# Kernel tuning notes

Measured on AMD Instinct MI355X. Metric: run time of the kernel, lower is better.

## Reference

```python
import jax, jax.numpy as jnp
import numpy as np

B, T, E, H = 2, 2048, 1024, 16
HD = E // H
EPS = 1e-5


def layer_norm(x, g, b):
    mu = jnp.mean(x, axis=-1, keepdims=True)
    var = jnp.mean(jnp.square(x - mu), axis=-1, keepdims=True)
    return (x - mu) * jax.lax.rsqrt(var + EPS) * g + b


def setup_inputs() -> dict:
    key = jax.random.key(0)
    ks = jax.random.split(key, 12)
    s = 0.02
    return {
        "x": jax.random.normal(ks[0], (B, T, E), jnp.float32),
        "Wk": jax.random.normal(ks[1], (E, E), jnp.float32) * s,
        "Wq": jax.random.normal(ks[2], (E, E), jnp.float32) * s,
        "Wv": jax.random.normal(ks[3], (E, E), jnp.float32) * s,
        "Wp": jax.random.normal(ks[4], (E, E), jnp.float32) * s,
        "bp": jnp.zeros((E,), jnp.float32),
        "W1": jax.random.normal(ks[5], (E, 4 * E), jnp.float32) * s,
        "b1": jnp.zeros((4 * E,), jnp.float32),
        "W2": jax.random.normal(ks[6], (4 * E, E), jnp.float32) * s,
        "b2": jnp.zeros((E,), jnp.float32),
        "g1": jnp.ones((E,), jnp.float32),
        "be1": jnp.zeros((E,), jnp.float32),
        "g2": jnp.ones((E,), jnp.float32),
        "be2": jnp.zeros((E,), jnp.float32),
    }


def reference(x, Wk, Wq, Wv, Wp, bp, W1, b1, W2, b2, g1, be1, g2, be2):
    # --- attention sublayer ---
    h = layer_norm(x, g1, be1)
    q = (h @ Wq).reshape(B, T, H, HD).transpose(0, 2, 1, 3)  # [B,H,T,HD]
    k = (h @ Wk).reshape(B, T, H, HD).transpose(0, 2, 1, 3)
    v = (h @ Wv).reshape(B, T, H, HD).transpose(0, 2, 1, 3)
    scores = jnp.einsum('bhqd,bhkd->bhqk', q, k) * (HD ** -0.5)
    causal = jnp.tril(jnp.ones((T, T), bool))
    scores = jnp.where(causal, scores, -jnp.inf)
    probs = jax.nn.softmax(scores, axis=-1)  # dropout is identity (eval)
    attn = jnp.einsum('bhqk,bhkd->bhqd', probs, v)
    attn = attn.transpose(0, 2, 1, 3).reshape(B, T, E)
    x = x + attn @ Wp + bp
    # --- FFN sublayer ---
    h2 = layer_norm(x, g2, be2)
    ff = jax.nn.relu(h2 @ W1 + b1) @ W2 + b2
    return x + ff
```

## Files before the change

### kernel.cpp

```cpp
#include <hip/hip_runtime.h>
#include <hip/hip_bf16.h>

#define B_ 2
#define T_ 2048
#define E_ 1024
#define H_ 16
#define HD_ 64
#define NT (B_*T_)

typedef __attribute__((ext_vector_type(8))) short s16x8;
typedef __attribute__((ext_vector_type(4))) float f32x4;
typedef __attribute__((ext_vector_type(4))) unsigned int u32x4;

using bf16 = __hip_bfloat16;

#define MFMA16(a,b,c) __builtin_amdgcn_mfma_f32_16x16x32_bf16(a,b,c,0,0,0)

__device__ inline unsigned short f2bf(float f) {
    bf16 h = __float2bfloat16(f);
    return *reinterpret_cast<unsigned short*>(&h);
}

__device__ __forceinline__ void async_cp16(const void* g, void* l) {
    __builtin_amdgcn_global_load_lds((const __attribute__((address_space(1))) void*)g,
                                     (__attribute__((address_space(3))) void*)l,
                                     16, 0, 0);
}

__global__ __launch_bounds__(256) void transpose_cvt4(const float* __restrict__ W0,
                                                      const float* __restrict__ W1,
                                                      const float* __restrict__ W2,
                                                      const float* __restrict__ W3,
                                                      bf16* __restrict__ Wt) {
    __shared__ float tile[32][33];
    int tx = threadIdx.x, ty = threadIdx.y;
    int z = blockIdx.z;
    const float* W = z == 0 ? W0 : z == 1 ? W1 : z == 2 ? W2 : W3;
    bf16* dst = Wt + (size_t)z * 1024 * 1024;
    int n0 = blockIdx.x * 32, k0 = blockIdx.y * 32;
#pragma unroll
    for (int i = 0; i < 4; ++i)
        tile[ty + i*8][tx] = W[(size_t)(k0 + ty + i*8)*1024 + n0 + tx];
    __syncthreads();
#pragma unroll
    for (int i = 0; i < 4; ++i)
        dst[(size_t)(n0 + ty + i*8)*1024 + k0 + tx] = __float2bfloat16(tile[tx][ty + i*8]);
}

__global__ __launch_bounds__(256) void transpose_cvt(const float* __restrict__ W,
                                                     bf16* __restrict__ Wt,
                                                     int K, int N) {
    __shared__ float tile[32][33];
    int tx = threadIdx.x, ty = threadIdx.y;
    int n0 = blockIdx.x * 32, k0 = blockIdx.y * 32;
#pragma unroll
    for (int i = 0; i < 4; ++i)
        tile[ty + i*8][tx] = W[(size_t)(k0 + ty + i*8)*N + n0 + tx];
    __syncthreads();
#pragma unroll
    for (int i = 0; i < 4; ++i)
        Wt[(size_t)(n0 + ty + i*8)*K + k0 + tx] = __float2bfloat16(tile[tx][ty + i*8]);
}

__global__ __launch_bounds__(256) void ln_kernel(const float* __restrict__ x,
                                                 const float* __restrict__ g,
                                                 const float* __restrict__ b,
                                                 bf16* __restrict__ h) {
    int row = blockIdx.x;
    int tid = threadIdx.x;
    const float4 xv = *reinterpret_cast<const float4*>(x + (size_t)row*E_ + tid*4);
    float s  = xv.x + xv.y + xv.z + xv.w;
    float sq = xv.x*xv.x + xv.y*xv.y + xv.z*xv.z + xv.w*xv.w;
#pragma unroll
    for (int o = 32; o > 0; o >>= 1) { s += __shfl_xor(s, o); sq += __shfl_xor(sq, o); }
    __shared__ float red[8];
    int w = tid >> 6, lane = tid & 63;
    if (lane == 0) { red[w] = s; red[4 + w] = sq; }
    __syncthreads();
    float S = red[0] + red[1] + red[2] + red[3];
    float Q = red[4] + red[5] + red[6] + red[7];
    float mu = S * (1.0f/E_);
    float var = Q * (1.0f/E_) - mu*mu;
    float rs = rsqrtf(var + 1e-5f);
    const float4 gv = *reinterpret_cast<const float4*>(g + tid*4);
    const float4 bv = *reinterpret_cast<const float4*>(b + tid*4);
    ushort4 o4;
    o4.x = f2bf((xv.x - mu)*rs*gv.x + bv.x);
    o4.y = f2bf((xv.y - mu)*rs*gv.y + bv.y);
    o4.z = f2bf((xv.z - mu)*rs*gv.z + bv.z);
    o4.w = f2bf((xv.w - mu)*rs*gv.w + bv.w);
    *reinterpret_cast<ushort4*>(h + (size_t)row*E_ + tid*4) = o4;
}

template<int BN, int EPI>
__global__ __launch_bounds__(256)
void gemm_t(const bf16* __restrict__ A, const bf16* __restrict__ Bt, void* Cout,
            const float* __restrict__ bias, const float* res,
            int M, int N, int K) {
    constexpr int NB = BN / 32;
    constexpr int HALF = BN / 2;
    __shared__ bf16 As[128*64];
    __shared__ bf16 Bs[BN*64];
    int tid = threadIdx.x;
    int lane = tid & 63, w = tid >> 6;
    int wr = w >> 1, wc = w & 1;
    int m0 = blockIdx.y * 128, n0 = blockIdx.x * BN;
    int lr = lane & 15, lq = lane >> 4;
    f32x4 acc[4][NB] = {};
    int srow = w*8 + (lane >> 3);
    int schunk = ((lane & 7) ^ (srow & 7)) * 8;
    const bf16* Ap = A  + (size_t)(m0 + srow)*K + schunk;
    const bf16* Bp = Bt + (size_t)(n0 + srow)*K + schunk;
    for (int k0 = 0; k0 < K; k0 += 64) {
#pragma unroll
        for (int i = 0; i < 4; ++i)
            async_cp16(Ap + (size_t)(i*32)*K + k0, (char*)As + i*4096 + w*1024);
#pragma unroll
        for (int i = 0; i < BN/32; ++i)
            async_cp16(Bp + (size_t)(i*32)*K + k0, (char*)Bs + i*4096 + w*1024);
        __syncthreads();
        const char* Asb = (const char*)As;
        const char* Bsb = (const char*)Bs;
        s16x8 af[2][4], bfr[2][NB];
#pragma unroll
        for (int m = 0; m < 4; ++m) {
            int row = wr*64 + m*16 + lr;
            int base = row*128, sw = (row & 7) << 4;
#pragma unroll
            for (int kk = 0; kk < 2; ++kk)
                af[kk][m] = *reinterpret_cast<const s16x8*>(Asb + base + ((kk*64 + lq*16) ^ sw));
        }
#pragma unroll
        for (int n = 0; n < NB; ++n) {
            int row = wc*HALF + n*16 + lr;
            int base = row*128, sw = (row & 7) << 4;
#pragma unroll
            for (int kk = 0; kk < 2; ++kk)
                bfr[kk][n] = *reinterpret_cast<const s16x8*>(Bsb + base + ((kk*64 + lq*16) ^ sw));
        }
        __builtin_amdgcn_s_setprio(1);
#pragma unroll
        for (int kk = 0; kk < 2; ++kk)
#pragma unroll
            for (int m = 0; m < 4; ++m)
#pragma unroll
                for (int n = 0; n < NB; ++n)
                    acc[m][n] = MFMA16(af[kk][m], bfr[kk][n], acc[m][n]);
        __builtin_amdgcn_s_setprio(0);
        __syncthreads();
    }
#pragma unroll
    for (int m = 0; m < 4; ++m) {
#pragma unroll
        for (int n = 0; n < NB; ++n) {
            int col = n0 + wc*HALF + n*16 + lr;
#pragma unroll
            for (int r = 0; r < 4; ++r) {
                int row = m0 + wr*64 + m*16 + lq*4 + r;
                float v = acc[m][n][r];
                if (EPI == 0) {
                    reinterpret_cast<bf16*>(Cout)[(size_t)row*N + col] = __float2bfloat16(v);
                } else if (EPI == 1) {
                    reinterpret_cast<float*>(Cout)[(size_t)row*N + col] =
                        v + bias[col] + res[(size_t)row*N + col];
                } else {
                    v += bias[col];
                    v = v > 0.f ? v : 0.f;
                    reinterpret_cast<bf16*>(Cout)[(size_t)row*N + col] = __float2bfloat16(v);
                }
            }
        }
    }
}

__global__ __launch_bounds__(256) void v_transpose(const bf16* __restrict__ qkv,
                                                   bf16* __restrict__ Vt) {
    __shared__ unsigned short tile[32][33];
    int tx = threadIdx.x, ty = threadIdx.y;
    int bh = blockIdx.z;
    int b = bh >> 4, h = bh & 15;
    int t0 = blockIdx.x * 32, d0 = blockIdx.y * 32;
    const unsigned short* src = reinterpret_cast<const unsigned short*>(qkv);
#pragma unroll
    for (int i = 0; i < 4; ++i)
        tile[ty + i*8][tx] = src[(size_t)(b*T_ + t0 + ty + i*8)*3072 + 2048 + h*64 + d0 + tx];
    __syncthreads();
    unsigned short* dst = reinterpret_cast<unsigned short*>(Vt);
#pragma unroll
    for (int i = 0; i < 4; ++i)
        dst[(size_t)(bh*64 + d0 + ty + i*8)*T_ + t0 + tx] = tile[tx][ty + i*8];
}

__global__ __launch_bounds__(256)
void flash_attn(const bf16* __restrict__ qkv, const bf16* __restrict__ Vt,
                bf16* __restrict__ O) {
    __shared__ char smem[40960];
    int tid = threadIdx.x;
    int lane = tid & 63, w = tid >> 6;
    int lr = lane & 15, lq = lane >> 4;
    int bh = blockIdx.y, b = bh >> 4, h = bh & 15;
    int qt = (int)((blockIdx.x + blockIdx.y) & 31);
    int q0 = qt * 64;
    int qw = q0 + w * 16;
    const bf16* Qb = qkv + (size_t)(b*T_)*3072 + h*HD_;
    const bf16* Kb = Qb + 1024;
    const bf16* Vb = Vt + (size_t)bh * HD_ * T_;
    char* Pw = smem + 32768 + w*2048;

    int sc_   = (((lane & 7) ^ ((lane >> 3) & 7))) * 8;
    int srow_ = w*8 + (lane >> 3);

    s16x8 qf[2];
#pragma unroll
    for (int kk = 0; kk < 2; ++kk)
        qf[kk] = *reinterpret_cast<const s16x8*>(Qb + (size_t)(qw + lr)*3072 + kk*32 + lq*8);
    f32x4 od[4] = {};
    float mrun = -1e30f, lrun = 0.f;
    const float SLOG2E = 0.125f * 1.44269504088896f;
    int ntiles = qt + 1;

#define STAGE(bufi, tile) do {                                                          \
        int kv0s_ = (tile) * 64;                                                        \
        _Pragma("unroll")                                                               \
        for (int i_ = 0; i_ < 2; ++i_) {                                                \
            int rr_ = i_*32 + srow_;                                                    \
            async_cp16(Kb + (size_t)(kv0s_ + rr_)*3072 + sc_,                           \
                       smem + (bufi)*8192 + i_*4096 + w*1024);                          \
            async_cp16(Vb + (size_t)rr_*2048 + kv0s_ + sc_,                             \
                       smem + 16384 + (bufi)*8192 + i_*4096 + w*1024);                  \
        } } while (0)

    STAGE(0, 0);
    for (int it = 0; it < ntiles; ++it) {
        int curb = it & 1;
        int kv0 = it * 64;
        if (it + 1 < ntiles) {
            STAGE(curb ^ 1, it + 1);
            asm volatile("s_waitcnt vmcnt(4)" ::: "memory");
        } else {
            asm volatile("s_waitcnt vmcnt(0)" ::: "memory");
        }
        __builtin_amdgcn_sched_barrier(0);
        __builtin_amdgcn_s_barrier();
        __builtin_amdgcn_sched_barrier(0);
        const char* Kt = smem + curb*8192;
        const char* Vtl = smem + 16384 + curb*8192;
        f32x4 sc[4];
        __builtin_amdgcn_s_setprio(1);
#pragma unroll
        for (int n = 0; n < 4; ++n) {
            int row = n*16 + lr;
            s16x8 kf0 = *reinterpret_cast<const s16x8*>(Kt + row*128 + ((lq ^ (row&7)) << 4));
            s16x8 kf1 = *reinterpret_cast<const s16x8*>(Kt + row*128 + (((4+lq) ^ (row&7)) << 4));
            f32x4 z = {0.f, 0.f, 0.f, 0.f};
            z = MFMA16(kf0, qf[0], z);
            z = MFMA16(kf1, qf[1], z);
            sc[n] = z;
        }
        __builtin_amdgcn_s_setprio(0);
        if (it == ntiles - 1) {
            int q = qw + lr;
#pragma unroll
            for (int n = 0; n < 4; ++n)
#pragma unroll
                for (int r = 0; r < 4; ++r)
                    if (kv0 + n*16 + lq*4 + r > q) sc[n][r] = -1e30f;
        }
        float mx01 = fmaxf(fmaxf(sc[0][0], sc[0][1]), fmaxf(sc[0][2], sc[0][3]));
        float mx1  = fmaxf(fmaxf(sc[1][0], sc[1][1]), fmaxf(sc[1][2], sc[1][3]));
        float mx2  = fmaxf(fmaxf(sc[2][0], sc[2][1]), fmaxf(sc[2][2], sc[2][3]));
        float mx3  = fmaxf(fmaxf(sc[3][0], sc[3][1]), fmaxf(sc[3][2], sc[3][3]));
        float pmax = fmaxf(fmaxf(mx01, mx1), fmaxf(mx2, mx3));
        pmax = fmaxf(pmax, __shfl_xor(pmax, 16));
        pmax = fmaxf(pmax, __shfl_xor(pmax, 32));
        float ps = pmax * SLOG2E;
        if (__ballot(ps > mrun + 8.f)) {
            float mn = fmaxf(mrun, ps);
            float corr = exp2f(mrun - mn);
            mrun = mn;
            lrun *= corr;
            float cR[4];
#pragma unroll
            for (int r = 0; r < 4; ++r) cR[r] = __shfl(corr, lq*4 + r);
#pragma unroll
            for (int nd = 0; nd < 4; ++nd)
#pragma unroll
                for (int r = 0; r < 4; ++r)
                    od[nd][r] *= cR[r];
        }
        float psum = 0.f;
#pragma unroll
        for (int n = 0; n < 4; ++n) {
            float p0 = exp2f(fmaf(sc[n][0], SLOG2E, -mrun));
            float p1 = exp2f(fmaf(sc[n][1], SLOG2E, -mrun));
            float p2 = exp2f(fmaf(sc[n][2], SLOG2E, -mrun));
            float p3 = exp2f(fmaf(sc[n][3], SLOG2E, -mrun));
            psum += (p0 + p1) + (p2 + p3);
            uint2 pk;
            pk.x = ((unsigned)f2bf(p1) << 16) | f2bf(p0);
            pk.y = ((unsigned)f2bf(p3) << 16) | f2bf(p2);
            int bo = (lr*128 + n*32 + lq*8) ^ ((lr & 7) << 4);
            *reinterpret_cast<uint2*>(Pw + bo) = pk;
        }
        psum += __shfl_xor(psum, 16);
        psum += __shfl_xor(psum, 32);
        lrun += psum;
        asm volatile("" ::: "memory");
        s16x8 pa[2];
#pragma unroll
        for (int kk = 0; kk < 2; ++kk) {
            int bo = (lr*128 + kk*64 + lq*16) ^ ((lr & 7) << 4);
            pa[kk] = *reinterpret_cast<const s16x8*>(Pw + bo);
        }
        __builtin_amdgcn_s_setprio(1);
#pragma unroll
        for (int nd = 0; nd < 4; ++nd) {
            int row = nd*16 + lr;
            s16x8 vf0 = *reinterpret_cast<const s16x8*>(Vtl + row*128 + ((lq ^ (row&7)) << 4));
            s16x8 vf1 = *reinterpret_cast<const s16x8*>(Vtl + row*128 + (((4+lq) ^ (row&7)) << 4));
            od[nd] = MFMA16(pa[0], vf0, od[nd]);
            od[nd] = MFMA16(pa[1], vf1, od[nd]);
        }
        __builtin_amdgcn_s_setprio(0);
        __builtin_amdgcn_sched_barrier(0);
        __builtin_amdgcn_s_barrier();
        __builtin_amdgcn_sched_barrier(0);
    }
#undef STAGE
    float lR[4];
#pragma unroll
    for (int r = 0; r < 4; ++r) lR[r] = 1.0f / __shfl(lrun, lq*4 + r);
#pragma unroll
    for (int nd = 0; nd < 4; ++nd) {
#pragma unroll
        for (int r = 0; r < 4; ++r) {
            int row = qw + lq*4 + r;
            O[(size_t)(b*T_ + row)*E_ + h*HD_ + nd*16 + lr] = __float2bfloat16(od[nd][r] * lR[r]);
        }
    }
}

extern "C" void kernel_launch(void* const* d_in, const int* in_sizes, int n_in,
                              void* d_out, int out_size, void* d_ws, size_t ws_size,
                              hipStream_t stream) {
    const float* x   = (const float*)d_in[0];
    const float* Wk  = (const float*)d_in[1];
    const float* Wq  = (const float*)d_in[2];
    const float* Wv  = (const float*)d_in[3];
    const float* Wp  = (const float*)d_in[4];
    const float* bp  = (const float*)d_in[5];
    const float* W1  = (const float*)d_in[6];
    const float* b1  = (const float*)d_in[7];
    const float* W2  = (const float*)d_in[8];
    const float* b2  = (const float*)d_in[9];
    const float* g1  = (const float*)d_in[10];
    const float* be1 = (const float*)d_in[11];
    const float* g2  = (const float*)d_in[12];
    const float* be2 = (const float*)d_in[13];
    float* out = (float*)d_out;

    char* ws = (char*)d_ws;
    bf16* Wqkv_t = (bf16*)(ws + 0);
    bf16* Wp_t   = (bf16*)(ws + 6291456);
    bf16* W1_t   = (bf16*)(ws + 8388608);
    bf16* W2_t   = (bf16*)(ws + 16777216);
    bf16* h      = (bf16*)(ws + 25165824);
    bf16* qkv    = (bf16*)(ws + 33554432);
    bf16* Vt     = (bf16*)(ws + 58720256);
    bf16* attnO  = (bf16*)(ws + 67108864);
    bf16* ff1    = (bf16*)(ws + 33554432);
    float* x2    = (ws_size >= 92274688) ? (float*)(ws + 75497472) : out;

    dim3 tb(32, 8);
    transpose_cvt4<<<dim3(32, 32, 4), tb, 0, stream>>>(Wq, Wk, Wv, Wp, Wqkv_t);
    transpose_cvt<<<dim3(128, 32), tb, 0, stream>>>(W1, W1_t, 1024, 4096);
    transpose_cvt<<<dim3(32, 128), tb, 0, stream>>>(W2, W2_t, 4096, 1024);

    ln_kernel<<<NT, 256, 0, stream>>>(x, g1, be1, h);
    gemm_t<128,0><<<dim3(24, 32), 256, 0, stream>>>(h, Wqkv_t, qkv, nullptr, nullptr, NT, 3072, 1024);
    v_transpose<<<dim3(64, 2, 32), tb, 0, stream>>>(qkv, Vt);
    flash_attn<<<dim3(32, 32), 256, 0, stream>>>(qkv, Vt, attnO);
    gemm_t<64,1><<<dim3(16, 32), 256, 0, stream>>>(attnO, Wp_t, x2, bp, x, NT, 1024, 1024);
    ln_kernel<<<NT, 256, 0, stream>>>(x2, g2, be2, h);
    gemm_t<128,2><<<dim3(32, 32), 256, 0, stream>>>(h, W1_t, ff1, b1, nullptr, NT, 4096, 1024);
    gemm_t<64,1><<<dim3(16, 32), 256, 0, stream>>>(ff1, W2_t, out, b2, x2, NT, 1024, 4096);
}
```

Before: 240.2 us.

## Pair complementary causal query tiles per flash-attention block and merge weight transposes

Each flash-attention block now handles two query tiles, qt and 31-qt, so every block does the same amount of causal work and shares each staged K/V tile between both query tiles. The grid is halved and LDS grows to hold a second P buffer. This is meant to remove load imbalance across the causal triangle and repeated K/V loads, at the cost of more registers and fewer blocks in flight. The change also merges the three weight transpose launches into one and uses a packed bf16 convert instruction for P.

```diff
diff --git a/kernel.cpp b/kernel.cpp
--- a/kernel.cpp
+++ b/kernel.cpp
@@ -21,45 +21,50 @@
     return *reinterpret_cast<unsigned short*>(&h);
 }
 
+__device__ __forceinline__ unsigned cvt_pk_bf16(float lo, float hi) {
+    unsigned r;
+    asm("v_cvt_pk_bf16_f32 %0, %1, %2" : "=v"(r) : "v"(lo), "v"(hi));
+    return r;
+}
+
 __device__ __forceinline__ void async_cp16(const void* g, void* l) {
     __builtin_amdgcn_global_load_lds((const __attribute__((address_space(1))) void*)g,
                                      (__attribute__((address_space(3))) void*)l,
                                      16, 0, 0);
 }
 
-__global__ __launch_bounds__(256) void transpose_cvt4(const float* __restrict__ W0,
-                                                      const float* __restrict__ W1,
-                                                      const float* __restrict__ W2,
-                                                      const float* __restrict__ W3,
-                                                      bf16* __restrict__ Wt) {
+__global__ __launch_bounds__(256) void transpose_all(const float* __restrict__ Wq,
+                                                     const float* __restrict__ Wk,
+                                                     const float* __restrict__ Wv,
+                                                     const float* __restrict__ Wp,
+                                                     const float* __restrict__ W1,
+                                                     const float* __restrict__ W2,
+                                                     bf16* __restrict__ Wqkv_t,
+                                                     bf16* __restrict__ W1_t,
+                                                     bf16* __restrict__ W2_t) {
     __shared__ float tile[32][33];
+    int id = blockIdx.x;
+    const float* src; bf16* dst; int K, N, n0, k0;
+    if (id < 4096) {
+        int z = id >> 10, t = id & 1023;
+        src = z == 0 ? Wq : z == 1 ? Wk : z == 2 ? Wv : Wp;
+        dst = Wqkv_t + (size_t)z * 1048576;
+        K = 1024; N = 1024; n0 = (t & 31) * 32; k0 = (t >> 5) * 32;
+    } else if (id < 8192) {
+        int t = id - 4096; src = W1; dst = W1_t; K = 1024; N = 4096;
+        n0 = (t & 127) * 32; k0 = (t >> 7) * 32;
+    } else {
+        int t = id - 8192; src = W2; dst = W2_t; K = 4096; N = 1024;
+        n0 = (t & 31) * 32; k0 = (t >> 5) * 32;
+    }
     int tx = threadIdx.x, ty = threadIdx.y;
-    int z = blockIdx.z;
-    const float* W = z == 0 ? W0 : z == 1 ? W1 : z == 2 ? W2 : W3;
-    bf16* dst = Wt + (size_t)z * 1024 * 1024;
-    int n0 = blockIdx.x * 32, k0 = blockIdx.y * 32;
 #pragma unroll
     for (int i = 0; i < 4; ++i)
-        tile[ty + i*8][tx] = W[(size_t)(k0 + ty + i*8)*1024 + n0 + tx];
+        tile[ty + i*8][tx] = src[(size_t)(k0 + ty + i*8)*N + n0 + tx];
     __syncthreads();
 #pragma unroll
     for (int i = 0; i < 4; ++i)
-        dst[(size_t)(n0 + ty + i*8)*1024 + k0 + tx] = __float2bfloat16(tile[tx][ty + i*8]);
-}
-
-__global__ __launch_bounds__(256) void transpose_cvt(const float* __restrict__ W,
-                                                     bf16* __restrict__ Wt,
-                                                     int K, int N) {
-    __shared__ float tile[32][33];
-    int tx = threadIdx.x, ty = threadIdx.y;
-    int n0 = blockIdx.x * 32, k0 = blockIdx.y * 32;
-#pragma unroll
-    for (int i = 0; i < 4; ++i)
-        tile[ty + i*8][tx] = W[(size_t)(k0 + ty + i*8)*N + n0 + tx];
-    __syncthreads();
-#pragma unroll
-    for (int i = 0; i < 4; ++i)
-        Wt[(size_t)(n0 + ty + i*8)*K + k0 + tx] = __float2bfloat16(tile[tx][ty + i*8]);
+        dst[(size_t)(n0 + ty + i*8)*K + k0 + tx] = __float2bfloat16(tile[tx][ty + i*8]);
 }
 
 __global__ __launch_bounds__(256) void ln_kernel(const float* __restrict__ x,
@@ -194,30 +199,118 @@
 __global__ __launch_bounds__(256)
 void flash_attn(const bf16* __restrict__ qkv, const bf16* __restrict__ Vt,
                 bf16* __restrict__ O) {
-    __shared__ char smem[40960];
+    __shared__ char smem[49152];
     int tid = threadIdx.x;
     int lane = tid & 63, w = tid >> 6;
     int lr = lane & 15, lq = lane >> 4;
     int bh = blockIdx.y, b = bh >> 4, h = bh & 15;
-    int qt = (int)((blockIdx.x + blockIdx.y) & 31);
-    int q0 = qt * 64;
-    int qw = q0 + w * 16;
+    int c = (int)((blockIdx.x + bh) & 15);
+    int qtA = (bh & 16) ? (15 - c) : c;
+    int qtB = 31 - qtA;
+    int ntB = qtB + 1;
+    int qwA = qtA*64 + w*16, qwB = qtB*64 + w*16;
     const bf16* Qb = qkv + (size_t)(b*T_)*3072 + h*HD_;
     const bf16* Kb = Qb + 1024;
     const bf16* Vb = Vt + (size_t)bh * HD_ * T_;
-    char* Pw = smem + 32768 + w*2048;
+    char* PwA = smem + 32768 + w*2048;
+    char* PwB = smem + 40960 + w*2048;
 
     int sc_   = (((lane & 7) ^ ((lane >> 3) & 7))) * 8;
     int srow_ = w*8 + (lane >> 3);
 
-    s16x8 qf[2];
-#pragma unroll
-    for (int kk = 0; kk < 2; ++kk)
-        qf[kk] = *reinterpret_cast<const s16x8*>(Qb + (size_t)(qw + lr)*3072 + kk*32 + lq*8);
-    f32x4 od[4] = {};
-    float mrun = -1e30f, lrun = 0.f;
+    s16x8 qfA[2], qfB[2];
+#pragma unroll
+    for (int kk = 0; kk < 2; ++kk) {
+        qfA[kk] = *reinterpret_cast<const s16x8*>(Qb + (size_t)(qwA + lr)*3072 + kk*32 + lq*8);
+        qfB[kk] = *reinterpret_cast<const s16x8*>(Qb + (size_t)(qwB + lr)*3072 + kk*32 + lq*8);
+    }
+    f32x4 odA[4] = {}, odB[4] = {};
+    float mA = -1e30f, lA = 0.f, mB = -1e30f, lB = 0.f;
     const float SLOG2E = 0.125f * 1.44269504088896f;
-    int ntiles = qt + 1;
+
+    auto step = [&](f32x4 (&od)[4], float& mrun, float& lrun, char* Pw,
+                    const s16x8 (&qf)[2], int qw, bool diag,
+                    const char* Kt, const char* Vtl, int kv0) {
+        f32x4 sc[4];
+        __builtin_amdgcn_s_setprio(1);
+#pragma unroll
+        for (int n = 0; n < 4; ++n) {
+            int row = n*16 + lr;
+            int ko = row*128 + ((lq ^ (row & 7)) << 4);
+            s16x8 kf0 = *reinterpret_cast<const s16x8*>(Kt + ko);
+            s16x8 kf1 = *reinterpret_cast<const s16x8*>(Kt + (ko ^ 64));
+            f32x4 z = {0.f, 0.f, 0.f, 0.f};
+            z = MFMA16(kf0, qf[0], z);
+            z = MFMA16(kf1, qf[1], z);
+            sc[n] = z;
+        }
+        __builtin_amdgcn_s_setprio(0);
+        if (diag) {
+            int q = qw + lr;
+#pragma unroll
+            for (int n = 0; n < 4; ++n)
+#pragma unroll
+                for (int r = 0; r < 4; ++r)
+                    if (kv0 + n*16 + lq*4 + r > q) sc[n][r] = -1e30f;
+        }
+        float mx0 = fmaxf(fmaxf(sc[0][0], sc[0][1]), fmaxf(sc[0][2], sc[0][3]));
+        float mx1 = fmaxf(fmaxf(sc[1][0], sc[1][1]), fmaxf(sc[1][2], sc[1][3]));
+        float mx2 = fmaxf(fmaxf(sc[2][0], sc[2][1]), fmaxf(sc[2][2], sc[2][3]));
+        float mx3 = fmaxf(fmaxf(sc[3][0], sc[3][1]), fmaxf(sc[3][2], sc[3][3]));
+        float pmax = fmaxf(fmaxf(mx0, mx1), fmaxf(mx2, mx3));
+        pmax = fmaxf(pmax, __shfl_xor(pmax, 16));
+        pmax = fmaxf(pmax, __shfl_xor(pmax, 32));
+        float ps = pmax * SLOG2E;
+        if (__ballot(ps > mrun + 8.f)) {
+            float mn = fmaxf(mrun, ps);
+            float corr = exp2f(mrun - mn);
+            mrun = mn;
+            lrun *= corr;
+            float cR[4];
+#pragma unroll
+            for (int r = 0; r < 4; ++r) cR[r] = __shfl(corr, lq*4 + r);
+#pragma unroll
+            for (int nd = 0; nd < 4; ++nd)
+#pragma unroll
+                for (int r = 0; r < 4; ++r)
+                    od[nd][r] *= cR[r];
+        }
+        float psum = 0.f;
+#pragma unroll
+        for (int n = 0; n < 4; ++n) {
+            float p0 = exp2f(fmaf(sc[n][0], SLOG2E, -mrun));
+            float p1 = exp2f(fmaf(sc[n][1], SLOG2E, -mrun));
+            float p2 = exp2f(fmaf(sc[n][2], SLOG2E, -mrun));
+            float p3 = exp2f(fmaf(sc[n][3], SLOG2E, -mrun));
+            psum += (p0 + p1) + (p2 + p3);
+            uint2 pk;
+            pk.x = cvt_pk_bf16(p0, p1);
+            pk.y = cvt_pk_bf16(p2, p3);
+            int bo = (lr*128 + n*32 + lq*8) ^ ((lr & 7) << 4);
+            *reinterpret_cast<uint2*>(Pw + bo) = pk;
+        }
+        psum += __shfl_xor(psum, 16);
+        psum += __shfl_xor(psum, 32);
+        lrun += psum;
+        asm volatile("" ::: "memory");
+        s16x8 pa[2];
+#pragma unroll
+        for (int kk = 0; kk < 2; ++kk) {
+            int bo = (lr*128 + kk*64 + lq*16) ^ ((lr & 7) << 4);
+            pa[kk] = *reinterpret_cast<const s16x8*>(Pw + bo);
+        }
+        __builtin_amdgcn_s_setprio(1);
+#pragma unroll
+        for (int nd = 0; nd < 4; ++nd) {
+            int row = nd*16 + lr;
+            int vo = row*128 + ((lq ^ (row & 7)) << 4);
+            s16x8 vf0 = *reinterpret_cast<const s16x8*>(Vtl + vo);
+            s16x8 vf1 = *reinterpret_cast<const s16x8*>(Vtl + (vo ^ 64));
+            od[nd] = MFMA16(pa[0], vf0, od[nd]);
+            od[nd] = MFMA16(pa[1], vf1, od[nd]);
+        }
+        __builtin_amdgcn_s_setprio(0);
+    };
 
 #define STAGE(bufi, tile) do {                                                          \
         int kv0s_ = (tile) * 64;                                                        \
@@ -231,10 +324,10 @@
         } } while (0)
 
     STAGE(0, 0);
-    for (int it = 0; it < ntiles; ++it) {
+    for (int it = 0; it < ntB; ++it) {
         int curb = it & 1;
         int kv0 = it * 64;
-        if (it + 1 < ntiles) {
+        if (it + 1 < ntB) {
             STAGE(curb ^ 1, it + 1);
             asm volatile("s_waitcnt vmcnt(4)" ::: "memory");
         } else {
@@ -245,97 +338,29 @@
         __builtin_amdgcn_sched_barrier(0);
         const char* Kt = smem + curb*8192;
         const char* Vtl = smem + 16384 + curb*8192;
-        f32x4 sc[4];
-        __builtin_amdgcn_s_setprio(1);
-#pragma unroll
-        for (int n = 0; n < 4; ++n) {
-            int row = n*16 + lr;
-            s16x8 kf0 = *reinterpret_cast<const s16x8*>(Kt + row*128 + ((lq ^ (row&7)) << 4));
-            s16x8 kf1 = *reinterpret_cast<const s16x8*>(Kt + row*128 + (((4+lq) ^ (row&7)) << 4));
-            f32x4 z = {0.f, 0.f, 0.f, 0.f};
-            z = MFMA16(kf0, qf[0], z);
-            z = MFMA16(kf1, qf[1], z);
-            sc[n] = z;
-        }
-        __builtin_amdgcn_s_setprio(0);
-        if (it == ntiles - 1) {
-            int q = qw + lr;
-#pragma unroll
-            for (int n = 0; n < 4; ++n)
-#pragma unroll
-                for (int r = 0; r < 4; ++r)
-                    if (kv0 + n*16 + lq*4 + r > q) sc[n][r] = -1e30f;
-        }
-        float mx01 = fmaxf(fmaxf(sc[0][0], sc[0][1]), fmaxf(sc[0][2], sc[0][3]));
-        float mx1  = fmaxf(fmaxf(sc[1][0], sc[1][1]), fmaxf(sc[1][2], sc[1][3]));
-        float mx2  = fmaxf(fmaxf(sc[2][0], sc[2][1]), fmaxf(sc[2][2], sc[2][3]));
-        float mx3  = fmaxf(fmaxf(sc[3][0], sc[3][1]), fmaxf(sc[3][2], sc[3][3]));
-        float pmax = fmaxf(fmaxf(mx01, mx1), fmaxf(mx2, mx3));
-        pmax = fmaxf(pmax, __shfl_xor(pmax, 16));
-        pmax = fmaxf(pmax, __shfl_xor(pmax, 32));
-        float ps = pmax * SLOG2E;
-        if (__ballot(ps > mrun + 8.f)) {
-            float mn = fmaxf(mrun, ps);
-            float corr = exp2f(mrun - mn);
-            mrun = mn;
-            lrun *= corr;
-            float cR[4];
-#pragma unroll
-            for (int r = 0; r < 4; ++r) cR[r] = __shfl(corr, lq*4 + r);
-#pragma unroll
-            for (int nd = 0; nd < 4; ++nd)
-#pragma unroll
-                for (int r = 0; r < 4; ++r)
-                    od[nd][r] *= cR[r];
-        }
-        float psum = 0.f;
-#pragma unroll
-        for (int n = 0; n < 4; ++n) {
-            float p0 = exp2f(fmaf(sc[n][0], SLOG2E, -mrun));
-            float p1 = exp2f(fmaf(sc[n][1], SLOG2E, -mrun));
-            float p2 = exp2f(fmaf(sc[n][2], SLOG2E, -mrun));
-            float p3 = exp2f(fmaf(sc[n][3], SLOG2E, -mrun));
-            psum += (p0 + p1) + (p2 + p3);
-            uint2 pk;
-            pk.x = ((unsigned)f2bf(p1) << 16) | f2bf(p0);
-            pk.y = ((unsigned)f2bf(p3) << 16) | f2bf(p2);
-            int bo = (lr*128 + n*32 + lq*8) ^ ((lr & 7) << 4);
-            *reinterpret_cast<uint2*>(Pw + bo) = pk;
-        }
-        psum += __shfl_xor(psum, 16);
-        psum += __shfl_xor(psum, 32);
-        lrun += psum;
-        asm volatile("" ::: "memory");
-        s16x8 pa[2];
-#pragma unroll
-        for (int kk = 0; kk < 2; ++kk) {
-            int bo = (lr*128 + kk*64 + lq*16) ^ ((lr & 7) << 4);
-            pa[kk] = *reinterpret_cast<const s16x8*>(Pw + bo);
-        }
-        __builtin_amdgcn_s_setprio(1);
-#pragma unroll
-        for (int nd = 0; nd < 4; ++nd) {
-            int row = nd*16 + lr;
-            s16x8 vf0 = *reinterpret_cast<const s16x8*>(Vtl + row*128 + ((lq ^ (row&7)) << 4));
-            s16x8 vf1 = *reinterpret_cast<const s16x8*>(Vtl + row*128 + (((4+lq) ^ (row&7)) << 4));
-            od[nd] = MFMA16(pa[0], vf0, od[nd]);
-            od[nd] = MFMA16(pa[1], vf1, od[nd]);
-        }
-        __builtin_amdgcn_s_setprio(0);
+        step(odB, mB, lB, PwB, qfB, qwB, it == qtB, Kt, Vtl, kv0);
+        if (it <= qtA)
+            step(odA, mA, lA, PwA, qfA, qwA, it == qtA, Kt, Vtl, kv0);
         __builtin_amdgcn_sched_barrier(0);
         __builtin_amdgcn_s_barrier();
         __builtin_amdgcn_sched_barrier(0);
     }
 #undef STAGE
-    float lR[4];
-#pragma unroll
-    for (int r = 0; r < 4; ++r) lR[r] = 1.0f / __shfl(lrun, lq*4 + r);
+    float lRA[4], lRB[4];
+#pragma unroll
+    for (int r = 0; r < 4; ++r) {
+        lRA[r] = 1.0f / __shfl(lA, lq*4 + r);
+        lRB[r] = 1.0f / __shfl(lB, lq*4 + r);
+    }
 #pragma unroll
     for (int nd = 0; nd < 4; ++nd) {
 #pragma unroll
         for (int r = 0; r < 4; ++r) {
-            int row = qw + lq*4 + r;
-            O[(size_t)(b*T_ + row)*E_ + h*HD_ + nd*16 + lr] = __float2bfloat16(od[nd][r] * lR[r]);
+            int rowA = qwA + lq*4 + r;
+            int rowB = qwB + lq*4 + r;
+            int col = h*HD_ + nd*16 + lr;
+            O[(size_t)(b*T_ + rowA)*E_ + col] = __float2bfloat16(odA[nd][r] * lRA[r]);
+            O[(size_t)(b*T_ + rowB)*E_ + col] = __float2bfloat16(odB[nd][r] * lRB[r]);
         }
     }
 }
@@ -372,14 +397,12 @@
     float* x2    = (ws_size >= 92274688) ? (float*)(ws + 75497472) : out;
 
     dim3 tb(32, 8);
-    transpose_cvt4<<<dim3(32, 32, 4), tb, 0, stream>>>(Wq, Wk, Wv, Wp, Wqkv_t);
-    transpose_cvt<<<dim3(128, 32), tb, 0, stream>>>(W1, W1_t, 1024, 4096);
-    transpose_cvt<<<dim3(32, 128), tb, 0, stream>>>(W2, W2_t, 4096, 1024);
+    transpose_all<<<12288, tb, 0, stream>>>(Wq, Wk, Wv, Wp, W1, W2, Wqkv_t, W1_t, W2_t);
 
     ln_kernel<<<NT, 256, 0, stream>>>(x, g1, be1, h);
     gemm_t<128,0><<<dim3(24, 32), 256, 0, stream>>>(h, Wqkv_t, qkv, nullptr, nullptr, NT, 3072, 1024);
     v_transpose<<<dim3(64, 2, 32), tb, 0, stream>>>(qkv, Vt);
-    flash_attn<<<dim3(32, 32), 256, 0, stream>>>(qkv, Vt, attnO);
+    flash_attn<<<dim3(16, 32), 256, 0, stream>>>(qkv, Vt, attnO);
     gemm_t<64,1><<<dim3(16, 32), 256, 0, stream>>>(attnO, Wp_t, x2, bp, x, NT, 1024, 1024);
     ln_kernel<<<NT, 256, 0, stream>>>(x2, g2, be2, h);
     gemm_t<128,2><<<dim3(32, 32), 256, 0, stream>>>(h, W1_t, ff1, b1, nullptr, NT, 4096, 1024);
```

After: 229.7 us. 4.4% less time.
